# Kernel tuning notes

Measured on AMD Instinct MI355X. Metric: run time of the kernel, lower is better.

Reference implementation:

```python
import jax, jax.numpy as jnp
import numpy as np

B, S, D, H = 2, 2048, 1024, 16
HD = D // H  # head dim = 64


def setup_inputs() -> dict:
    key0 = jax.random.key(0)
    ks = jax.random.split(key0, 12)
    scale = 1.0 / np.sqrt(D)
    inp = {
        "query": jax.random.normal(ks[0], (B, S, D), jnp.float32),
        "key": jax.random.normal(ks[1], (B, S, D), jnp.float32),
        "value": jax.random.normal(ks[2], (B, S, D), jnp.float32),
        "mask": jax.random.randint(ks[3], (B, S), 0, 2, jnp.int32),
        "Wq": jax.random.normal(ks[4], (D, D), jnp.float32) * scale,
        "bq": jnp.zeros((D,), jnp.float32),
        "Wk": jax.random.normal(ks[5], (D, D), jnp.float32) * scale,
        "bk": jnp.zeros((D,), jnp.float32),
        "Wv": jax.random.normal(ks[6], (D, D), jnp.float32) * scale,
        "bv": jnp.zeros((D,), jnp.float32),
        "Wo": jax.random.normal(ks[7], (D, D), jnp.float32) * scale,
        "bo": jnp.zeros((D,), jnp.float32),
    }
    return inp


def _split_heads(x):  # (B,S,D) -> (B,H,S,HD)
    Bb, Ss, Dd = x.shape
    return x.reshape(Bb, Ss, H, HD).transpose(0, 2, 1, 3)


def reference(query, key, value, mask, Wq, bq, Wk, bk, Wv, bv, Wo, bo):
    # Linear projections (torch Linear: x @ W.T + b), split into heads.
    q = _split_heads(query @ Wq.T + bq)
    k = _split_heads(key @ Wk.T + bk)
    v = _split_heads(value @ Wv.T + bv)
    # Scaled dot-product scores: (B,H,S,S); NOTE: original divides by sqrt(head_dim).
    scores = jnp.einsum("bhqd,bhkd->bhqk", q, k) / np.sqrt(HD).astype(np.float32)
    # mask (B,S) masks KEY positions; broadcast over heads and query positions.
    scores = jnp.where(mask[:, None, None, :] == 0, jnp.float32(-1e9), scores)
    attn = jax.nn.softmax(scores, axis=-1)
    # Dropout is identity in eval mode.
    x = jnp.einsum("bhqk,bhkd->bhqd", attn, v)  # (B,H,S,HD)
    x = x.transpose(0, 2, 1, 3).reshape(query.shape[0], query.shape[1], D)
    return x @ Wo.T + bo
```

## Files before the change

kernel.cpp:

```cpp
#include <hip/hip_runtime.h>
#include <hip/hip_bf16.h>
#include <hip/hip_fp16.h>

#define BB 2
#define SS 2048
#define DD 1024
#define HH 16
#define HD 64
#define MM (BB * SS)

typedef __attribute__((ext_vector_type(8))) _Float16 half8;
typedef __attribute__((ext_vector_type(4))) float f32x4;
typedef __attribute__((ext_vector_type(4))) short short4v;

static __device__ __forceinline__ short f2h(float f) {
    _Float16 h = (_Float16)f;
    return __builtin_bit_cast(short, h);
}

static __device__ __forceinline__ unsigned pk2(float a, float b) {
    auto h = __builtin_amdgcn_cvt_pkrtz(a, b);
    return __builtin_bit_cast(unsigned, h);
}

static __device__ __forceinline__ float fexp2(float x) {
    return __builtin_amdgcn_exp2f(x);
}

static __device__ __forceinline__ void gload16(const void* g, void* l) {
    __builtin_amdgcn_global_load_lds(
        (const __attribute__((address_space(1))) unsigned*)g,
        (__attribute__((address_space(3))) unsigned*)l, 16, 0, 0);
}

#define SC2E 0.18033688011112042f

__global__ __launch_bounds__(256) void cvt_kernel(
    const float* __restrict__ wq, const float* __restrict__ wk,
    const float* __restrict__ wv, const float* __restrict__ wo,
    const int* __restrict__ mask,
    short* __restrict__ wq16, short* __restrict__ wk16,
    short* __restrict__ wv16, short* __restrict__ wo16,
    short* __restrict__ mask16)
{
    const int i = (blockIdx.x * 256 + threadIdx.x) * 4;
    if (blockIdx.y == 4) {
        if (i >= BB * SS) return;
        const int4 mi = *(const int4*)&mask[i];
        short4v f;
        f.x = f2h(mi.x ? 1.0f : 0.0f);
        f.y = f2h(mi.y ? 1.0f : 0.0f);
        f.z = f2h(mi.z ? 1.0f : 0.0f);
        f.w = f2h(mi.w ? 1.0f : 0.0f);
        *(short4v*)&mask16[i] = f;
        return;
    }
    const float* src; short* dst;
    switch (blockIdx.y) {
        case 0: src = wq; dst = wq16; break;
        case 1: src = wk; dst = wk16; break;
        case 2: src = wv; dst = wv16; break;
        default: src = wo; dst = wo16; break;
    }
    if (i >= DD * DD) return;
    const float4 f = *(const float4*)&src[i];
    short4v h;
    h.x = f2h(f.x); h.y = f2h(f.y); h.z = f2h(f.z); h.w = f2h(f.w);
    *(short4v*)&dst[i] = h;
}

template<bool AFP32>
static __device__ __forceinline__ void gemm_phase(
    const short* __restrict__ AsCur, const short* __restrict__ BsCur,
    char* AsNxt, char* BsNxt,
    const void* __restrict__ A, const short* __restrict__ W,
    int m0, int n0, int k_next, bool do_stage,
    int t, int lr, int lq, int wc,
    f32x4 acc[4][2])
{
    constexpr int WN = 32;
    constexpr int NI = 2;
    const int K = DD;

    float4 af32[4];
    if (do_stage) {
        #pragma unroll
        for (int c = 0; c < 4; ++c) {
            const int b = c * 4096 + t * 16;
            const int row = b >> 7;
            const int coff = b & 127;
            const int scoff = coff ^ ((row & 7) << 4);
            gload16((const char*)W + ((size_t)(n0 + row) * K + k_next) * 2 + scoff,
                    BsNxt + b);
        }
        #pragma unroll
        for (int c = 0; c < 2; ++c) {
            const int b = c * 4096 + t * 16;
            const int row = b >> 7;
            const int coff = b & 127;
            if constexpr (AFP32) {
                const float* ap = (const float*)A +
                    (size_t)(m0 + row) * K + k_next + (coff >> 1);
                af32[c * 2]     = *(const float4*)ap;
                af32[c * 2 + 1] = *(const float4*)(ap + 4);
            } else {
                const int scoff = coff ^ ((row & 7) << 4);
                gload16((const char*)A + ((size_t)(m0 + row) * K + k_next) * 2 + scoff,
                        AsNxt + b);
            }
        }
    }

    half8 af[4][2], bf[NI][2];
    #pragma unroll
    for (int mi = 0; mi < 4; ++mi) {
        const int row = mi * 16 + lr;
        #pragma unroll
        for (int ks = 0; ks < 2; ++ks) {
            const int col = (ks * 32 + lq * 8) ^ ((row & 7) << 3);
            af[mi][ks] = *(const half8*)&AsCur[row * 64 + col];
        }
    }
    #pragma unroll
    for (int ni = 0; ni < NI; ++ni) {
        const int row = wc * WN + ni * 16 + lr;
        #pragma unroll
        for (int ks = 0; ks < 2; ++ks) {
            const int col = (ks * 32 + lq * 8) ^ ((row & 7) << 3);
            bf[ni][ks] = *(const half8*)&BsCur[row * 64 + col];
        }
    }
    __builtin_amdgcn_s_setprio(1);
    #pragma unroll
    for (int ks = 0; ks < 2; ++ks)
        #pragma unroll
        for (int mi = 0; mi < 4; ++mi)
            #pragma unroll
            for (int ni = 0; ni < NI; ++ni)
                acc[mi][ni] = __builtin_amdgcn_mfma_f32_16x16x32_f16(
                    af[mi][ks], bf[ni][ks], acc[mi][ni], 0, 0, 0);
    __builtin_amdgcn_s_setprio(0);

    if (do_stage) {
        if constexpr (AFP32) {
            #pragma unroll
            for (int c = 0; c < 2; ++c) {
                const int b = c * 4096 + t * 16;
                const int row = b >> 7;
                const int coff = b & 127;
                uint4 pv;
                pv.x = pk2(af32[c * 2].x,     af32[c * 2].y);
                pv.y = pk2(af32[c * 2].z,     af32[c * 2].w);
                pv.z = pk2(af32[c * 2 + 1].x, af32[c * 2 + 1].y);
                pv.w = pk2(af32[c * 2 + 1].z, af32[c * 2 + 1].w);
                *(uint4*)(AsNxt + row * 128 + (coff ^ ((row & 7) << 4))) = pv;
            }
        }
    }

    __syncthreads();
}

template<bool AFP32>
__global__ __launch_bounds__(256) void gemm_f16(
    const void* __restrict__ A0, const void* __restrict__ A1, const void* __restrict__ A2,
    const short* __restrict__ W0, const short* __restrict__ W1, const short* __restrict__ W2,
    const float* __restrict__ b0, const float* __restrict__ b1, const float* __restrict__ b2,
    void* __restrict__ C0, void* __restrict__ C1, void* __restrict__ C2,
    int mode0, int mode1, int mode2,
    float os0, float os1, float os2,
    const int* __restrict__ mask)
{
    constexpr int TM = 64;
    constexpr int WN = 32;
    constexpr int NI = 2;

    const int gx = gridDim.x, gy = gridDim.y;
    const int total = gx * gy * gridDim.z;
    const int lin = (blockIdx.z * gy + blockIdx.y) * gx + blockIdx.x;
    const int work = (lin & 7) * (total >> 3) + (lin >> 3);
    const int z = work / (gx * gy);
    const int r0 = work % (gx * gy);
    const int bx = r0 / gy;
    const int by = r0 % gy;

    const void* A = (z == 0) ? A0 : (z == 1) ? A1 : A2;
    const short* W = (z == 0) ? W0 : (z == 1) ? W1 : W2;
    const float* bias = (z == 0) ? b0 : (z == 1) ? b1 : b2;
    void* C = (z == 0) ? C0 : (z == 1) ? C1 : C2;
    const int mode = (z == 0) ? mode0 : (z == 1) ? mode1 : mode2;
    const float os = (z == 0) ? os0 : (z == 1) ? os1 : os2;

    __shared__ short Asw[2][TM * 64];
    __shared__ short Bsw[2][128 * 64];

    const int t = threadIdx.x;
    const int wave = t >> 6, lane = t & 63;
    const int lr = lane & 15, lq = lane >> 4;
    const int wc = wave;
    const int m0 = bx * TM, n0 = by * 128;
    const int K = DD;

    f32x4 acc[4][NI] = {};

    {
        #pragma unroll
        for (int c = 0; c < 4; ++c) {
            const int b = c * 4096 + t * 16;
            const int row = b >> 7;
            const int coff = b & 127;
            const int scoff = coff ^ ((row & 7) << 4);
            gload16((const char*)W + ((size_t)(n0 + row) * K) * 2 + scoff,
                    (char*)Bsw[0] + b);
        }
        #pragma unroll
        for (int c = 0; c < 2; ++c) {
            const int b = c * 4096 + t * 16;
            const int row = b >> 7;
            const int coff = b & 127;
            if constexpr (AFP32) {
                const float* ap = (const float*)A + (size_t)(m0 + row) * K + (coff >> 1);
                const float4 f0 = *(const float4*)ap;
                const float4 f1 = *(const float4*)(ap + 4);
                uint4 pv;
                pv.x = pk2(f0.x, f0.y);
                pv.y = pk2(f0.z, f0.w);
                pv.z = pk2(f1.x, f1.y);
                pv.w = pk2(f1.z, f1.w);
                *(uint4*)((char*)Asw[0] + row * 128 + (coff ^ ((row & 7) << 4))) = pv;
            } else {
                const int scoff = coff ^ ((row & 7) << 4);
                gload16((const char*)A + ((size_t)(m0 + row) * K) * 2 + scoff,
                        (char*)Asw[0] + b);
            }
        }
    }
    __syncthreads();

    for (int k0 = 0; k0 < K; k0 += 128) {
        gemm_phase<AFP32>(Asw[0], Bsw[0], (char*)Asw[1], (char*)Bsw[1],
                          A, W, m0, n0, k0 + 64, true,
                          t, lr, lq, wc, acc);
        gemm_phase<AFP32>(Asw[1], Bsw[1], (char*)Asw[0], (char*)Bsw[0],
                          A, W, m0, n0, k0 + 128, (k0 + 128) < K,
                          t, lr, lq, wc, acc);
    }

    if (mode == 2) {
        #pragma unroll
        for (int mi = 0; mi < 4; ++mi) {
            const int m = m0 + mi * 16 + lq * 4;
            const int bidx = m >> 11;
            const int s = m & (SS - 1);
            const int4 mk = *(const int4*)&mask[m];
            const float m0f = mk.x ? 1.0f : 0.0f;
            const float m1f = mk.y ? 1.0f : 0.0f;
            const float m2f = mk.z ? 1.0f : 0.0f;
            const float m3f = mk.w ? 1.0f : 0.0f;
            #pragma unroll
            for (int ni = 0; ni < NI; ++ni) {
                const int n = n0 + wc * WN + ni * 16 + lr;
                const int h = n >> 6, d = n & (HD - 1);
                const float bi = bias[n];
                short4v pv;
                pv.x = f2h((acc[mi][ni][0] + bi) * m0f);
                pv.y = f2h((acc[mi][ni][1] + bi) * m1f);
                pv.z = f2h((acc[mi][ni][2] + bi) * m2f);
                pv.w = f2h((acc[mi][ni][3] + bi) * m3f);
                *(short4v*)&((short*)C)[(((size_t)bidx * HH + h) * HD + d) * SS + s] = pv;
            }
        }
    } else {
        #pragma unroll
        for (int mi = 0; mi < 4; ++mi) {
            #pragma unroll
            for (int r = 0; r < 4; ++r) {
                const int m = m0 + mi * 16 + lq * 4 + r;
                const int bidx = m >> 11;
                const int s = m & (SS - 1);
                #pragma unroll
                for (int ni = 0; ni < NI; ++ni) {
                    const int n = n0 + wc * WN + ni * 16 + lr;
                    const float val = (acc[mi][ni][r] + bias[n]) * os;
                    if (mode == 0) {
                        ((float*)C)[(size_t)m * DD + n] = val;
                    } else {
                        const int h = n >> 6, d = n & (HD - 1);
                        ((short*)C)[(((size_t)bidx * HH + h) * SS + s) * HD + d] = f2h(val);
                    }
                }
            }
        }
    }
}

static __device__ __forceinline__ void attn_tile_body(
    const short* __restrict__ Ks, const short* __restrict__ Vts,
    char* KsN, char* VtsN,
    const char* kb, const char* vb,
    int kv_stage, bool do_stage,
    const short* __restrict__ mrow, int kv0,
    const half8 qf[2], short* Pw,
    int t, int lr, int lq,
    f32x4 o[4], f32x4& ol)
{
    if (do_stage) {
        #pragma unroll
        for (int c = 0; c < 2; ++c) {
            const int off = c * 4096 + t * 16;
            const int row = off >> 7, coff = off & 127;
            const int sw = coff ^ ((row & 7) << 4);
            gload16(kb + (size_t)(kv_stage + row) * 128 + sw, KsN + off);
            gload16(vb + (size_t)row * (SS * 2) + kv_stage * 2 + sw, VtsN + off);
        }
    }

    half8 mf[2];
    #pragma unroll
    for (int ks = 0; ks < 2; ++ks)
        mf[ks] = *(const half8*)&mrow[kv0 + ks * 32 + lq * 8];

    f32x4 sc[4] = {};
    __builtin_amdgcn_s_setprio(1);
    #pragma unroll
    for (int kt = 0; kt < 4; ++kt) {
        const int kr = kt * 16 + lr;
        #pragma unroll
        for (int ks = 0; ks < 2; ++ks) {
            half8 kf = *(const half8*)&Ks[kr * 64 + ((ks * 32 + lq * 8) ^ ((kr & 7) << 3))];
            sc[kt] = __builtin_amdgcn_mfma_f32_16x16x32_f16(kf, qf[ks], sc[kt], 0, 0, 0);
        }
    }
    __builtin_amdgcn_s_setprio(0);

    const int xsw = (lr & 7) << 3;
    #pragma unroll
    for (int kt = 0; kt < 4; ++kt) {
        const float p0 = fexp2(sc[kt][0]);
        const float p1 = fexp2(sc[kt][1]);
        const float p2 = fexp2(sc[kt][2]);
        const float p3 = fexp2(sc[kt][3]);
        const int cb = kt * 16 + lq * 4;
        uint2 pp;
        pp.x = pk2(p0, p1);
        pp.y = pk2(p2, p3);
        *(uint2*)&Pw[lr * 64 + (cb ^ xsw)] = pp;
    }

    half8 pf[2];
    #pragma unroll
    for (int ks = 0; ks < 2; ++ks)
        pf[ks] = *(const half8*)&Pw[lr * 64 + ((ks * 32 + lq * 8) ^ xsw)];
    __builtin_amdgcn_s_setprio(1);
    #pragma unroll
    for (int ks = 0; ks < 2; ++ks)
        ol = __builtin_amdgcn_mfma_f32_16x16x32_f16(pf[ks], mf[ks], ol, 0, 0, 0);
    #pragma unroll
    for (int dt = 0; dt < 4; ++dt) {
        const int dr = dt * 16 + lr;
        #pragma unroll
        for (int ks = 0; ks < 2; ++ks) {
            half8 vf = *(const half8*)&Vts[dr * 64 + ((ks * 32 + lq * 8) ^ ((dr & 7) << 3))];
            o[dt] = __builtin_amdgcn_mfma_f32_16x16x32_f16(pf[ks], vf, o[dt], 0, 0, 0);
        }
    }
    __builtin_amdgcn_s_setprio(0);

    __syncthreads();
}

__global__ __launch_bounds__(256) void attn_mfma_kernel(
    const short* __restrict__ q,
    const short* __restrict__ k,
    const short* __restrict__ vt,
    const short* __restrict__ mask16,
    short* __restrict__ x)
{
    const int lin = (blockIdx.z * HH + blockIdx.y) * (SS / 64) + blockIdx.x;
    const int swz = (lin & 7) * 128 + (lin >> 3);
    const int qt = swz & 31;
    const int hb = swz >> 5;
    const int h  = hb & (HH - 1);
    const int b  = hb >> 4;

    const int t = threadIdx.x;
    const int wave = t >> 6, lane = t & 63;
    const int lr = lane & 15;
    const int lq = lane >> 4;

    __shared__ short QPs[64 * 64];
    __shared__ short KsD[2][64 * 64];
    __shared__ short VtsD[2][64 * 64];

    const size_t base  = ((size_t)(b * HH + h)) * SS * HD;
    const size_t basev = ((size_t)(b * HH + h)) * HD * SS;
    const char* kb = (const char*)(k + base);
    const char* vb = (const char*)(vt + basev);

    {
        const char* qb = (const char*)(q + base + (size_t)qt * 64 * HD);
        #pragma unroll
        for (int c = 0; c < 2; ++c) {
            const int off = c * 4096 + t * 16;
            const int row = off >> 7, coff = off & 127;
            const int sw = coff ^ ((row & 7) << 4);
            gload16(qb + row * 128 + sw, (char*)QPs + off);
            gload16(kb + (size_t)row * 128 + sw, (char*)KsD[0] + off);
            gload16(vb + (size_t)row * (SS * 2) + sw, (char*)VtsD[0] + off);
        }
    }
    __syncthreads();

    half8 qf[2];
    #pragma unroll
    for (int ks = 0; ks < 2; ++ks) {
        const int r = wave * 16 + lr;
        qf[ks] = *(const half8*)&QPs[r * 64 + ((ks * 32 + lq * 8) ^ ((r & 7) << 3))];
    }
    __syncthreads();

    f32x4 o[4] = {};
    f32x4 ol = {};
    const short* mrow = &mask16[b * SS];
    short* Pw = &QPs[wave * 1024];

    for (int kv0 = 0; kv0 < SS; kv0 += 128) {
        attn_tile_body(KsD[0], VtsD[0], (char*)KsD[1], (char*)VtsD[1],
                       kb, vb, kv0 + 64, true,
                       mrow, kv0, qf, Pw, t, lr, lq, o, ol);
        attn_tile_body(KsD[1], VtsD[1], (char*)KsD[0], (char*)VtsD[0],
                       kb, vb, kv0 + 128, (kv0 + 128) < SS,
                       mrow, kv0 + 64, qf, Pw, t, lr, lq, o, ol);
    }

    float linv[4];
    #pragma unroll
    for (int r = 0; r < 4; ++r) linv[r] = 1.0f / ol[r];
    const int srow = qt * 64 + wave * 16;
    #pragma unroll
    for (int dt = 0; dt < 4; ++dt)
        #pragma unroll
        for (int r = 0; r < 4; ++r)
            x[((size_t)b * SS + srow + lq * 4 + r) * DD + h * HD + dt * 16 + lr] =
                f2h(o[dt][r] * linv[r]);
}

extern "C" void kernel_launch(void* const* d_in, const int* in_sizes, int n_in,
                              void* d_out, int out_size, void* d_ws, size_t ws_size,
                              hipStream_t stream) {
    const float* query = (const float*)d_in[0];
    const float* key   = (const float*)d_in[1];
    const float* value = (const float*)d_in[2];
    const int*   mask  = (const int*)d_in[3];
    const float* Wq = (const float*)d_in[4];
    const float* bq = (const float*)d_in[5];
    const float* Wk = (const float*)d_in[6];
    const float* bk = (const float*)d_in[7];
    const float* Wv = (const float*)d_in[8];
    const float* bv = (const float*)d_in[9];
    const float* Wo = (const float*)d_in[10];
    const float* bo = (const float*)d_in[11];
    float* out = (float*)d_out;

    const size_t NACT = (size_t)MM * DD;
    const size_t NW   = (size_t)DD * DD;
    short* wq16   = (short*)d_ws;
    short* wk16   = wq16 + NW;
    short* wv16   = wk16 + NW;
    short* wo16   = wv16 + NW;
    short* q_ws   = wo16 + NW;
    short* k_ws   = q_ws + NACT;
    short* vt_ws  = k_ws + NACT;
    short* mask16 = vt_ws + NACT;
    short* x16    = mask16 + BB * SS;

    cvt_kernel<<<dim3(NW / 4 / 256, 5), 256, 0, stream>>>(
        Wq, Wk, Wv, Wo, mask,
        wq16, wk16, wv16, wo16, mask16);

    gemm_f16<true><<<dim3(MM / 64, DD / 128, 3), 256, 0, stream>>>(
        query, key, value, wq16, wk16, wv16, bq, bk, bv,
        q_ws, k_ws, vt_ws, 1, 1, 2, SC2E, 1.0f, 1.0f, mask);

    attn_mfma_kernel<<<dim3(SS / 64, HH, BB), 256, 0, stream>>>(
        q_ws, k_ws, vt_ws, mask16, x16);

    gemm_f16<false><<<dim3(MM / 64, DD / 128, 1), 256, 0, stream>>>(
        x16, x16, x16, wo16, wo16, wo16, bo, bo, bo,
        out, out, out, 0, 0, 0, 1.0f, 1.0f, 1.0f, mask);
}
```

Before: 125.0 us.

## Compact unmasked keys to front and skip fully masked KV tiles in attention

A new partition kernel prefix-sums the key mask per batch and gives each position a compacted index, with unmasked keys placed first. The K and V projections scatter their outputs to these compacted positions, and the mask16 vector becomes a prefix mask. The attention loop then stops at the rounded-up count of unmasked keys instead of scanning all of S. With a random mask about half the KV tiles are skipped, at the cost of an extra small launch and scattered stores in the projection epilogue.

```diff
diff --git a/kernel.cpp b/kernel.cpp
--- a/kernel.cpp
+++ b/kernel.cpp
@@ -35,26 +35,46 @@
 
 #define SC2E 0.18033688011112042f
 
+__global__ __launch_bounds__(256) void partition_kernel(
+    const int* __restrict__ mask, int* __restrict__ cpos,
+    short* __restrict__ mask16, int* __restrict__ nu)
+{
+    const int b = blockIdx.x;
+    const int t = threadIdx.x;
+    __shared__ int sc[256];
+    const int* mrow = mask + b * SS;
+    int loc[8];
+    int cnt = 0;
+    #pragma unroll
+    for (int j = 0; j < 8; ++j) { loc[j] = (mrow[t * 8 + j] != 0); cnt += loc[j]; }
+    sc[t] = cnt;
+    __syncthreads();
+    for (int off = 1; off < 256; off <<= 1) {
+        const int v = sc[t];
+        const int va = (t >= off) ? sc[t - off] : 0;
+        __syncthreads();
+        sc[t] = v + va;
+        __syncthreads();
+    }
+    const int total = sc[255];
+    if (t == 0) nu[b] = total;
+    int u = sc[t] - cnt;
+    #pragma unroll
+    for (int j = 0; j < 8; ++j) {
+        const int s = t * 8 + j;
+        cpos[b * SS + s] = loc[j] ? u : (total + (s - u));
+        u += loc[j];
+        mask16[b * SS + s] = f2h((s < total) ? 1.0f : 0.0f);
+    }
+}
+
 __global__ __launch_bounds__(256) void cvt_kernel(
     const float* __restrict__ wq, const float* __restrict__ wk,
     const float* __restrict__ wv, const float* __restrict__ wo,
-    const int* __restrict__ mask,
     short* __restrict__ wq16, short* __restrict__ wk16,
-    short* __restrict__ wv16, short* __restrict__ wo16,
-    short* __restrict__ mask16)
+    short* __restrict__ wv16, short* __restrict__ wo16)
 {
     const int i = (blockIdx.x * 256 + threadIdx.x) * 4;
-    if (blockIdx.y == 4) {
-        if (i >= BB * SS) return;
-        const int4 mi = *(const int4*)&mask[i];
-        short4v f;
-        f.x = f2h(mi.x ? 1.0f : 0.0f);
-        f.y = f2h(mi.y ? 1.0f : 0.0f);
-        f.z = f2h(mi.z ? 1.0f : 0.0f);
-        f.w = f2h(mi.w ? 1.0f : 0.0f);
-        *(short4v*)&mask16[i] = f;
-        return;
-    }
     const float* src; short* dst;
     switch (blockIdx.y) {
         case 0: src = wq; dst = wq16; break;
@@ -169,7 +189,8 @@
     void* __restrict__ C0, void* __restrict__ C1, void* __restrict__ C2,
     int mode0, int mode1, int mode2,
     float os0, float os1, float os2,
-    const int* __restrict__ mask)
+    int perm0, int perm1, int perm2,
+    const int* __restrict__ mask, const int* __restrict__ cpos)
 {
     constexpr int TM = 64;
     constexpr int WN = 32;
@@ -190,6 +211,7 @@
     void* C = (z == 0) ? C0 : (z == 1) ? C1 : C2;
     const int mode = (z == 0) ? mode0 : (z == 1) ? mode1 : mode2;
     const float os = (z == 0) ? os0 : (z == 1) ? os1 : os2;
+    const int perm = (z == 0) ? perm0 : (z == 1) ? perm1 : perm2;
 
     __shared__ short Asw[2][TM * 64];
     __shared__ short Bsw[2][128 * 64];
@@ -249,25 +271,22 @@
     if (mode == 2) {
         #pragma unroll
         for (int mi = 0; mi < 4; ++mi) {
-            const int m = m0 + mi * 16 + lq * 4;
-            const int bidx = m >> 11;
-            const int s = m & (SS - 1);
-            const int4 mk = *(const int4*)&mask[m];
-            const float m0f = mk.x ? 1.0f : 0.0f;
-            const float m1f = mk.y ? 1.0f : 0.0f;
-            const float m2f = mk.z ? 1.0f : 0.0f;
-            const float m3f = mk.w ? 1.0f : 0.0f;
+            const int mbase = m0 + mi * 16 + lq * 4;
+            const int bidx = mbase >> 11;
+            const int4 mk = *(const int4*)&mask[mbase];
+            const int4 cp = *(const int4*)&cpos[mbase];
+            const float mmul[4] = { mk.x ? 1.0f : 0.0f, mk.y ? 1.0f : 0.0f,
+                                    mk.z ? 1.0f : 0.0f, mk.w ? 1.0f : 0.0f };
+            const int cpr[4] = { cp.x, cp.y, cp.z, cp.w };
             #pragma unroll
             for (int ni = 0; ni < NI; ++ni) {
                 const int n = n0 + wc * WN + ni * 16 + lr;
                 const int h = n >> 6, d = n & (HD - 1);
                 const float bi = bias[n];
-                short4v pv;
-                pv.x = f2h((acc[mi][ni][0] + bi) * m0f);
-                pv.y = f2h((acc[mi][ni][1] + bi) * m1f);
-                pv.z = f2h((acc[mi][ni][2] + bi) * m2f);
-                pv.w = f2h((acc[mi][ni][3] + bi) * m3f);
-                *(short4v*)&((short*)C)[(((size_t)bidx * HH + h) * HD + d) * SS + s] = pv;
+                short* cb = &((short*)C)[(((size_t)bidx * HH + h) * HD + d) * SS];
+                #pragma unroll
+                for (int r = 0; r < 4; ++r)
+                    cb[cpr[r]] = f2h((acc[mi][ni][r] + bi) * mmul[r]);
             }
         }
     } else {
@@ -277,7 +296,7 @@
             for (int r = 0; r < 4; ++r) {
                 const int m = m0 + mi * 16 + lq * 4 + r;
                 const int bidx = m >> 11;
-                const int s = m & (SS - 1);
+                const int s = (mode == 1 && perm) ? cpos[m] : (m & (SS - 1));
                 #pragma unroll
                 for (int ni = 0; ni < NI; ++ni) {
                     const int n = n0 + wc * WN + ni * 16 + lr;
@@ -374,6 +393,7 @@
     const short* __restrict__ k,
     const short* __restrict__ vt,
     const short* __restrict__ mask16,
+    const int* __restrict__ nu,
     short* __restrict__ x)
 {
     const int lin = (blockIdx.z * HH + blockIdx.y) * (SS / 64) + blockIdx.x;
@@ -397,6 +417,8 @@
     const char* kb = (const char*)(k + base);
     const char* vb = (const char*)(vt + basev);
 
+    const int limit = ((nu[b] + 63) >> 6) << 6;
+
     {
         const char* qb = (const char*)(q + base + (size_t)qt * 64 * HD);
         #pragma unroll
@@ -424,13 +446,14 @@
     const short* mrow = &mask16[b * SS];
     short* Pw = &QPs[wave * 1024];
 
-    for (int kv0 = 0; kv0 < SS; kv0 += 128) {
+    for (int kv0 = 0; kv0 < limit; kv0 += 128) {
         attn_tile_body(KsD[0], VtsD[0], (char*)KsD[1], (char*)VtsD[1],
-                       kb, vb, kv0 + 64, true,
+                       kb, vb, kv0 + 64, (kv0 + 64) < limit,
                        mrow, kv0, qf, Pw, t, lr, lq, o, ol);
-        attn_tile_body(KsD[1], VtsD[1], (char*)KsD[0], (char*)VtsD[0],
-                       kb, vb, kv0 + 128, (kv0 + 128) < SS,
-                       mrow, kv0 + 64, qf, Pw, t, lr, lq, o, ol);
+        if (kv0 + 64 < limit)
+            attn_tile_body(KsD[1], VtsD[1], (char*)KsD[0], (char*)VtsD[0],
+                           kb, vb, kv0 + 128, (kv0 + 128) < limit,
+                           mrow, kv0 + 64, qf, Pw, t, lr, lq, o, ol);
     }
 
     float linv[4];
@@ -473,19 +496,24 @@
     short* vt_ws  = k_ws + NACT;
     short* mask16 = vt_ws + NACT;
     short* x16    = mask16 + BB * SS;
-
-    cvt_kernel<<<dim3(NW / 4 / 256, 5), 256, 0, stream>>>(
-        Wq, Wk, Wv, Wo, mask,
-        wq16, wk16, wv16, wo16, mask16);
+    int*   cpos   = (int*)(x16 + NACT);
+    int*   nu     = cpos + BB * SS;
+
+    partition_kernel<<<dim3(BB), 256, 0, stream>>>(mask, cpos, mask16, nu);
+
+    cvt_kernel<<<dim3(NW / 4 / 256, 4), 256, 0, stream>>>(
+        Wq, Wk, Wv, Wo, wq16, wk16, wv16, wo16);
 
     gemm_f16<true><<<dim3(MM / 64, DD / 128, 3), 256, 0, stream>>>(
         query, key, value, wq16, wk16, wv16, bq, bk, bv,
-        q_ws, k_ws, vt_ws, 1, 1, 2, SC2E, 1.0f, 1.0f, mask);
+        q_ws, k_ws, vt_ws, 1, 1, 2, SC2E, 1.0f, 1.0f,
+        0, 1, 1, mask, cpos);
 
     attn_mfma_kernel<<<dim3(SS / 64, HH, BB), 256, 0, stream>>>(
-        q_ws, k_ws, vt_ws, mask16, x16);
+        q_ws, k_ws, vt_ws, mask16, nu, x16);
 
     gemm_f16<false><<<dim3(MM / 64, DD / 128, 1), 256, 0, stream>>>(
         x16, x16, x16, wo16, wo16, wo16, bo, bo, bo,
-        out, out, out, 0, 0, 0, 1.0f, 1.0f, 1.0f, mask);
-}
+        out, out, out, 0, 0, 0, 1.0f, 1.0f, 1.0f,
+        0, 0, 0, mask, cpos);
+}
```

Result: slower. 131.3 us (+5.1%).
